# Kernel tuning notes

Hardware: AMD Instinct MI355X
Metric: run time of the kernel (lower is better)

## Reference

```python
import jax, jax.numpy as jnp
import numpy as np

REF_MIC = 0
LOAD = 0.001 / np.sqrt(2.0)  # diagonal loading added to both real and imag parts


def _to_complex(x):
    # x: (N, 2, ...) real/imag stacked -> complex (N, ...)
    return x[:, 0] + 1j * x[:, 1]


def setup_inputs() -> dict:
    key = jax.random.key(0)
    k1, k2, k3 = jax.random.split(key, 3)
    N, C, T, F = 8, 16, 300, 257
    mixture = jax.random.normal(k1, (N, 2, C, T, F), dtype=jnp.float32)
    target = jax.random.normal(k2, (N, 2, C, T, F), dtype=jnp.float32)
    steering_vector = jax.random.normal(k3, (N, 2, C, F), dtype=jnp.float32)
    return {"mixture": mixture, "target": target, "steering_vector": steering_vector}


def reference(mixture, target, steering_vector):
    N, _, C, T, F = mixture.shape
    y = _to_complex(mixture)  # (N, C, T, F)
    x = _to_complex(target)   # (N, C, T, F)

    # Spatial covariance of mixture, mean over time frames (sum/T), fused einsum
    # phi[n,f] = (1/T) * sum_t y[n,:,t,f] y[n,:,t,f]^H  -> (N, F, C, C)
    phi = jnp.einsum('nctf,ndtf->nfcd', y, jnp.conj(y)) / T
    eye = jnp.eye(C, dtype=phi.dtype)
    # original adds load to BOTH real and imag diagonals (broadcast over RI dim)
    phi = phi + (LOAD + 1j * LOAD) * eye
    phi_inv = jnp.linalg.inv(phi)  # (N, F, C, C)

    # Cross covariance between mixture and reference-mic target
    A = jnp.transpose(y, (0, 3, 2, 1))            # (N, F, T, C)
    b = jnp.transpose(x[:, REF_MIC], (0, 2, 1))   # (N, F, T)
    mu_a = jnp.mean(A, axis=(0, 2), keepdims=True)  # mean over batch and time
    mu_b = jnp.mean(b, axis=(0, 2), keepdims=True)
    # mean over T of (A-mu_a)(b-mu_b)^H -> (N, F, C)
    phi_yx0 = jnp.mean((A - mu_a) * jnp.conj(b - mu_b)[..., None], axis=2)

    # MWF weights: w = phi_inv @ phi_yx0  -> (N, F, C)
    w = jnp.einsum('nfcd,nfd->nfc', phi_inv, phi_yx0)

    # Beamform: X_bf[n,t,f] = w[n,f]^H y[n,:,t,f]
    Xbf = jnp.einsum('nfc,nctf->ntf', jnp.conj(w), y)  # (N, T, F)

    # Back to real/imag stacked (N, 2, 1, T, F) matching torch output layout
    out = jnp.stack([Xbf.real, Xbf.imag], axis=1)[:, :, None]
    return out
```

## Files before the change

kernel.cpp:

```cpp
#include <hip/hip_runtime.h>

#define N_     8
#define C_     16
#define T_     300
#define F_     257
#define TF_    (T_*F_)
#define CTF_   (C_*TF_)
#define N2CTF_ (2*CTF_)

#define FT_    32
#define NFT_   9
#define TS_    5
#define SROW_  34
#define SSTG_  (SROW_*32)
#define SBUF_  (TS_*SSTG_)
#define NTILE_ 10
#define PHIC_  (NTILE_*16)

#define MREC_  272

#define LOADC  7.0710678118654755e-04f

typedef float v2f __attribute__((ext_vector_type(2)));

__device__ __forceinline__ float2 cmul(float2 a, float2 b) {
  return make_float2(a.x*b.x - a.y*b.y, a.x*b.y + a.y*b.x);
}
__device__ __forceinline__ float2 cmulc(float2 a, float2 b) {
  return make_float2(a.x*b.x + a.y*b.y, a.y*b.x - a.x*b.y);
}
__device__ __forceinline__ float2 cdiv(float2 a, float2 b) {
  float inv = 1.0f / (b.x*b.x + b.y*b.y);
  return make_float2((a.x*b.x + a.y*b.y)*inv, (a.y*b.x - a.x*b.y)*inv);
}
__device__ __forceinline__ float2 cadd(float2 a, float2 b){ return make_float2(a.x+b.x, a.y+b.y); }
__device__ __forceinline__ float2 csub(float2 a, float2 b){ return make_float2(a.x-b.x, a.y-b.y); }

__device__ __forceinline__ void gload4(const float* g, float* l) {
  __builtin_amdgcn_global_load_lds(
      (const __attribute__((address_space(1))) unsigned int*)g,
      (__attribute__((address_space(3))) unsigned int*)l, 4, 0, 0);
}

template<int TCH>
__global__ __launch_bounds__(320) void k1_cov(const float* __restrict__ mix,
                                              const float* __restrict__ tgt,
                                              float2* __restrict__ phi_pf,
                                              float2* __restrict__ syx_pf,
                                              float2* __restrict__ sy_pf,
                                              float2* __restrict__ sx_pf) {
  __shared__ float ys[2 * SBUF_];
  v2f* phi_p = (v2f*)phi_pf;
  v2f* syx_p = (v2f*)syx_pf;
  v2f* sy_p  = (v2f*)sy_pf;
  v2f* sx_p  = (v2f*)sx_pf;
  const int tid = threadIdx.x;
  const int ft = blockIdx.x, tc = blockIdx.y, n = blockIdx.z;
  const int fbase = ft * FT_;
  const int t0 = tc * TCH;
  const int fl = tid & 31;
  const int g  = tid >> 5;
  int ti = 0, tj = g;
  while (tj > ti) { ++ti; tj -= ti; }
  const int c0 = ti * 4;
  const int d0 = tj * 4;
  const bool sThread = (tj == 0);

  const int w     = tid >> 6;
  const int plane = (tid >> 5) & 1;
  const int f_ld  = min(fbase + fl, F_ - 1);

  const float* mixN = mix + n * N2CTF_;
  const float* tgtN = tgt + n * N2CTF_;
  const float* ysrc = mixN + plane * CTF_ + (t0 + w) * F_ + f_ld;
  const float* xsrc = tgtN + plane * CTF_ + (t0 + w) * F_ + f_ld;

  v2f acc[4][4];
  #pragma unroll
  for (int i = 0; i < 4; ++i)
    #pragma unroll
    for (int j = 0; j < 4; ++j) acc[i][j] = (v2f){0.f, 0.f};
  v2f syx[4], sy[4], sx = (v2f){0.f, 0.f};
  #pragma unroll
  for (int i = 0; i < 4; ++i) { syx[i] = (v2f){0.f,0.f}; sy[i] = (v2f){0.f,0.f}; }

  constexpr int NS = TCH / TS_;

  {
    float* dst = &ys[w * SSTG_];
    #pragma unroll
    for (int c = 0; c < 16; ++c) gload4(ysrc + c * TF_, dst + 2 * c * 32);
    gload4(xsrc, dst + 32 * 32);
  }

  for (int s = 0; s < NS; ++s) {
    __syncthreads();
    if (s + 1 < NS) {
      float* dst = &ys[((s + 1) & 1) * SBUF_ + w * SSTG_];
      const float* yp = ysrc + (s + 1) * (TS_ * F_);
      #pragma unroll
      for (int c = 0; c < 16; ++c) gload4(yp + c * TF_, dst + 2 * c * 32);
      gload4(xsrc + (s + 1) * (TS_ * F_), dst + 32 * 32);
    }
    const float* bufc = &ys[(s & 1) * SBUF_];
    #pragma unroll
    for (int tl = 0; tl < TS_; ++tl) {
      const float* rt = bufc + tl * SSTG_;
      v2f a[4], bu[4], bv[4];
      #pragma unroll
      for (int i = 0; i < 4; ++i) {
        float re = rt[(2 * (c0 + i)) * 32 + fl];
        float im = rt[(2 * (c0 + i)) * 32 + 32 + fl];
        a[i] = (v2f){re, im};
      }
      #pragma unroll
      for (int j = 0; j < 4; ++j) {
        float re = rt[(2 * (d0 + j)) * 32 + fl];
        float im = rt[(2 * (d0 + j)) * 32 + 32 + fl];
        bu[j] = (v2f){re, -im};
        bv[j] = (v2f){im,  re};
      }
      #pragma unroll
      for (int i = 0; i < 4; ++i)
        #pragma unroll
        for (int j = 0; j < 4; ++j)
          acc[i][j] += a[i].x * bu[j] + a[i].y * bv[j];
      if (sThread) {
        float xre = rt[32 * 32 + fl];
        float xim = rt[33 * 32 + fl];
        v2f xu = (v2f){xre, -xim};
        v2f xw = (v2f){xim,  xre};
        #pragma unroll
        for (int i = 0; i < 4; ++i) {
          syx[i] += a[i].x * xu + a[i].y * xw;
          sy[i]  += a[i];
        }
        if (g == 0) sx += (v2f){xre, xim};
      }
    }
  }

  const int f = fbase + fl;
  if (f < F_) {
    const int tcn = tc * N_ + n;
    v2f* pb = phi_p + ((size_t)tcn * F_ + f) * PHIC_ + g * 16;
    #pragma unroll
    for (int i = 0; i < 4; ++i)
      #pragma unroll
      for (int j = 0; j < 4; ++j) pb[i * 4 + j] = acc[i][j];
    if (sThread) {
      v2f* s1 = syx_p + ((size_t)tcn * F_ + f) * C_ + c0;
      v2f* s2 = sy_p  + ((size_t)tcn * F_ + f) * C_ + c0;
      #pragma unroll
      for (int i = 0; i < 4; ++i) { s1[i] = syx[i]; s2[i] = sy[i]; }
      if (g == 0) sx_p[(size_t)tcn * F_ + f] = sx;
    }
  }
}

template<int TCP>
__global__ __launch_bounds__(256) void k2a_reduce(const float2* __restrict__ phi_p,
                                                  const float2* __restrict__ syx_p,
                                                  const float2* __restrict__ sy_p,
                                                  const float2* __restrict__ sx_p,
                                                  float2* __restrict__ Mg) {
  __shared__ float2 ld_sy[TCP * N_ * C_];
  __shared__ float2 ld_syx[TCP * C_];
  __shared__ float2 ld_sx[TCP * N_];
  __shared__ float2 muB_s, sxO_s;
  const int f = blockIdx.x, n = blockIdx.y;
  const int tid = threadIdx.x;
  const int i = tid >> 4, j = tid & 15;

  const int ti = i >> 2, tj = j >> 2, ci = i & 3, cj = j & 3;
  int gL, cell; bool cj_flip;
  if (ti >= tj) { gL = ti * (ti + 1) / 2 + tj; cell = ci * 4 + cj; cj_flip = false; }
  else          { gL = tj * (tj + 1) / 2 + ti; cell = cj * 4 + ci; cj_flip = true; }
  const int off = gL * 16 + cell;

  float2 s = make_float2(0.f, 0.f);
  for (int tc = 0; tc < TCP; ++tc) {
    float2 v = phi_p[((size_t)(tc * N_ + n) * F_ + f) * PHIC_ + off];
    s.x += v.x; s.y += v.y;
  }
  if (cj_flip) s.y = -s.y;
  if (i == j) { s.x += (float)T_ * LOADC; s.y += (float)T_ * LOADC; }

  for (int idx = tid; idx < TCP * N_ * C_; idx += 256) {
    int tcn = idx >> 4, c = idx & 15;
    ld_sy[idx] = sy_p[((size_t)tcn * F_ + f) * C_ + c];
  }
  for (int idx = tid; idx < TCP * C_; idx += 256) {
    int tc = idx >> 4, c = idx & 15;
    ld_syx[idx] = syx_p[((size_t)(tc * N_ + n) * F_ + f) * C_ + c];
  }
  for (int idx = tid; idx < TCP * N_; idx += 256) {
    ld_sx[idx] = sx_p[(size_t)idx * F_ + f];
  }
  __syncthreads();

  float2 muA_r = make_float2(0.f,0.f), ownY = make_float2(0.f,0.f), ownYX = make_float2(0.f,0.f);
  if (tid < 16) {
    float2 allY = make_float2(0.f,0.f);
    for (int tcn = 0; tcn < TCP * N_; ++tcn) allY = cadd(allY, ld_sy[tcn * C_ + tid]);
    for (int tc = 0; tc < TCP; ++tc) {
      ownY  = cadd(ownY,  ld_sy[(tc * N_ + n) * C_ + tid]);
      ownYX = cadd(ownYX, ld_syx[tc * C_ + tid]);
    }
    const float invNT = 1.0f / ((float)N_ * (float)T_);
    muA_r = make_float2(allY.x * invNT, allY.y * invNT);
  }
  if (tid == 16) {
    float2 own = make_float2(0.f,0.f), all = make_float2(0.f,0.f);
    for (int tc = 0; tc < TCP; ++tc)
      for (int nn = 0; nn < N_; ++nn) {
        float2 v = ld_sx[tc * N_ + nn];
        all = cadd(all, v);
        if (nn == n) own = cadd(own, v);
      }
    const float invNT = 1.0f / ((float)N_ * (float)T_);
    muB_s = make_float2(all.x * invNT, all.y * invNT);
    sxO_s = own;
  }
  __syncthreads();

  float2* dst = Mg + (size_t)(n * F_ + f) * MREC_;
  dst[tid] = s;
  if (tid < 16) {
    float2 r = ownYX;
    r = csub(r, cmulc(muA_r, sxO_s));
    r = csub(r, cmulc(ownY, muB_s));
    float2 t3 = cmulc(muA_r, muB_s);
    r.x += (float)T_ * t3.x; r.y += (float)T_ * t3.y;
    dst[256 + tid] = r;
  }
}

__global__ __launch_bounds__(64) void k2b_solve(const float2* __restrict__ Mg,
                                                float* __restrict__ wre,
                                                float* __restrict__ wim) {
  __shared__ float2 M[16 * 17];
  const int f = blockIdx.x, n = blockIdx.y;
  const int tid = threadIdx.x;
  const float2* src = Mg + (size_t)(n * F_ + f) * MREC_;
  #pragma unroll
  for (int r = 0; r < 4; ++r) {
    int idx = tid + 64 * r;
    M[(idx >> 4) * 17 + (idx & 15)] = src[idx];
  }
  if (tid < 16) M[tid * 17 + 16] = src[256 + tid];
  __syncthreads();

  const int i = tid >> 2, q = tid & 3;
  for (int k = 0; k < 16; ++k) {
    float2 fac = cdiv(M[i * 17 + k], M[k * 17 + k]);
    __syncthreads();
    if (i != k) {
      #pragma unroll
      for (int jj = 0; jj < 4; ++jj) {
        int j = q * 4 + jj;
        M[i * 17 + j] = csub(M[i * 17 + j], cmul(fac, M[k * 17 + j]));
      }
      if (q == 3) M[i * 17 + 16] = csub(M[i * 17 + 16], cmul(fac, M[k * 17 + 16]));
    }
    __syncthreads();
  }
  if (q == 0) {
    float2 w = cdiv(M[i * 17 + 16], M[i * 17 + i]);
    wre[(n * C_ + i) * F_ + f] = w.x;
    wim[(n * C_ + i) * F_ + f] = w.y;
  }
}

__global__ __launch_bounds__(320) void k3_bf(const float* __restrict__ mix,
                                             const float* __restrict__ wre,
                                             const float* __restrict__ wim,
                                             float* __restrict__ out) {
  const int t0 = blockIdx.x * 2, n = blockIdx.y;
  const int f = threadIdx.x;
  if (f >= F_) return;
  const float* mixN = mix + n * N2CTF_;
  const float* wR = wre + n * C_ * F_;
  const float* wI = wim + n * C_ * F_;
  float* outN = out + n * 2 * TF_;
  float wr[16], wi[16];
  #pragma unroll
  for (int c = 0; c < 16; ++c) { wr[c] = wR[c * F_ + f]; wi[c] = wI[c * F_ + f]; }
  const float* yb = mixN + t0 * F_ + f;
  float xr0 = 0.f, xi0 = 0.f, xr1 = 0.f, xi1 = 0.f;
  #pragma unroll
  for (int c = 0; c < 16; ++c) {
    float yr0 = yb[c * TF_],      yi0 = yb[CTF_ + c * TF_];
    float yr1 = yb[c * TF_ + F_], yi1 = yb[CTF_ + c * TF_ + F_];
    xr0 += wr[c] * yr0 + wi[c] * yi0;
    xi0 += wr[c] * yi0 - wi[c] * yr0;
    xr1 += wr[c] * yr1 + wi[c] * yi1;
    xi1 += wr[c] * yi1 - wi[c] * yr1;
  }
  outN[t0 * F_ + f] = xr0;
  outN[TF_ + t0 * F_ + f] = xi0;
  outN[(t0 + 1) * F_ + f] = xr1;
  outN[TF_ + (t0 + 1) * F_ + f] = xi1;
}

template<int TCP>
static void launch_all(const float* mix, const float* tgt, float* ws, float* out,
                       hipStream_t stream) {
  constexpr int TCH = T_ / TCP;
  static_assert(TCH * TCP == T_ && TCH % TS_ == 0, "chunking");
  float2* phi_p = (float2*)ws;
  float2* syx_p = phi_p + (size_t)TCP * N_ * F_ * PHIC_;
  float2* sy_p  = syx_p + (size_t)TCP * N_ * F_ * C_;
  float2* sx_p  = sy_p  + (size_t)TCP * N_ * F_ * C_;
  float2* Mg    = sx_p  + (size_t)TCP * N_ * F_;
  float*  wre   = (float*)(Mg + (size_t)N_ * F_ * MREC_);
  float*  wim   = wre + N_ * C_ * F_;
  k1_cov<TCH><<<dim3(NFT_, TCP, N_), dim3(320), 0, stream>>>(mix, tgt, phi_p, syx_p, sy_p, sx_p);
  k2a_reduce<TCP><<<dim3(F_, N_), dim3(256), 0, stream>>>(phi_p, syx_p, sy_p, sx_p, Mg);
  k2b_solve<<<dim3(F_, N_), dim3(64), 0, stream>>>(Mg, wre, wim);
  k3_bf<<<dim3(T_ / 2, N_), dim3(320), 0, stream>>>(mix, wre, wim, out);
}

static size_t ws_need_bytes(int tcp) {
  size_t fl2 = (size_t)tcp * N_ * F_ * (PHIC_ + C_ + C_ + 1) + (size_t)N_ * F_ * MREC_;
  return fl2 * 8 + 2ull * N_ * C_ * F_ * 4;
}

extern "C" void kernel_launch(void* const* d_in, const int* in_sizes, int n_in,
                              void* d_out, int out_size, void* d_ws, size_t ws_size,
                              hipStream_t stream) {
  const float* mix = (const float*)d_in[0];
  const float* tgt = (const float*)d_in[1];
  float* out = (float*)d_out;
  float* ws  = (float*)d_ws;
  if (ws_size >= ws_need_bytes(10))      launch_all<10>(mix, tgt, ws, out, stream);
  else if (ws_size >= ws_need_bytes(6))  launch_all<6>(mix, tgt, ws, out, stream);
  else if (ws_size >= ws_need_bytes(2))  launch_all<2>(mix, tgt, ws, out, stream);
  else                                   launch_all<1>(mix, tgt, ws, out, stream);
}
```

Measured before the change: 220.9 us.

## Triple-buffer covariance loads, fuse reduce and solve kernels, drop TCP=10 path

The covariance kernel moves from double to triple buffering. It issues async global-to-LDS loads two stages ahead, with explicit vmcnt waits and barriers, so memory latency is hidden better. The reduce and Gauss-Jordan solve kernels are merged into one, which removes a global round-trip of the per-frequency matrix and one kernel launch. The solve now uses 256 threads with one element each instead of 64 threads. The TCP=10 configuration is dropped, likely because its stage count per chunk is too small for the ring, so the default is now TCP=6 with fewer blocks in k1.

```diff
diff --git a/kernel.cpp b/kernel.cpp
--- a/kernel.cpp
+++ b/kernel.cpp
@@ -14,10 +14,9 @@
 #define SROW_  34
 #define SSTG_  (SROW_*32)
 #define SBUF_  (TS_*SSTG_)
+#define NSLOT_ 3
 #define NTILE_ 10
 #define PHIC_  (NTILE_*16)
-
-#define MREC_  272
 
 #define LOADC  7.0710678118654755e-04f
 
@@ -49,7 +48,7 @@
                                               float2* __restrict__ syx_pf,
                                               float2* __restrict__ sy_pf,
                                               float2* __restrict__ sx_pf) {
-  __shared__ float ys[2 * SBUF_];
+  __shared__ float ys[NSLOT_ * SBUF_];
   v2f* phi_p = (v2f*)phi_pf;
   v2f* syx_p = (v2f*)syx_pf;
   v2f* sy_p  = (v2f*)sy_pf;
@@ -85,24 +84,32 @@
   for (int i = 0; i < 4; ++i) { syx[i] = (v2f){0.f,0.f}; sy[i] = (v2f){0.f,0.f}; }
 
   constexpr int NS = TCH / TS_;
-
-  {
-    float* dst = &ys[w * SSTG_];
+  static_assert(NS >= 3, "ring needs >=3 stages");
+
+  auto issue = [&](int stg) {
+    float* dst = &ys[(stg % NSLOT_) * SBUF_ + w * SSTG_];
+    const float* yp = ysrc + stg * (TS_ * F_);
     #pragma unroll
-    for (int c = 0; c < 16; ++c) gload4(ysrc + c * TF_, dst + 2 * c * 32);
-    gload4(xsrc, dst + 32 * 32);
-  }
+    for (int c = 0; c < 16; ++c) gload4(yp + c * TF_, dst + 2 * c * 32);
+    gload4(xsrc + stg * (TS_ * F_), dst + 32 * 32);
+  };
+
+  issue(0);
+  issue(1);
 
   for (int s = 0; s < NS; ++s) {
-    __syncthreads();
-    if (s + 1 < NS) {
-      float* dst = &ys[((s + 1) & 1) * SBUF_ + w * SSTG_];
-      const float* yp = ysrc + (s + 1) * (TS_ * F_);
-      #pragma unroll
-      for (int c = 0; c < 16; ++c) gload4(yp + c * TF_, dst + 2 * c * 32);
-      gload4(xsrc + (s + 1) * (TS_ * F_), dst + 32 * 32);
-    }
-    const float* bufc = &ys[(s & 1) * SBUF_];
+    if (s + 2 < NS) {
+      issue(s + 2);
+      asm volatile("s_waitcnt vmcnt(34)" ::: "memory");
+    } else if (s + 1 < NS) {
+      asm volatile("s_waitcnt vmcnt(17)" ::: "memory");
+    } else {
+      asm volatile("s_waitcnt vmcnt(0)" ::: "memory");
+    }
+    __builtin_amdgcn_sched_barrier(0);
+    __builtin_amdgcn_s_barrier();
+
+    const float* bufc = &ys[(s % NSLOT_) * SBUF_];
     #pragma unroll
     for (int tl = 0; tl < TS_; ++tl) {
       const float* rt = bufc + tl * SSTG_;
@@ -138,6 +145,9 @@
         if (g == 0) sx += (v2f){xre, xim};
       }
     }
+    asm volatile("s_waitcnt lgkmcnt(0)" ::: "memory");
+    __builtin_amdgcn_sched_barrier(0);
+    __builtin_amdgcn_s_barrier();
   }
 
   const int f = fbase + fl;
@@ -159,14 +169,16 @@
 }
 
 template<int TCP>
-__global__ __launch_bounds__(256) void k2a_reduce(const float2* __restrict__ phi_p,
-                                                  const float2* __restrict__ syx_p,
-                                                  const float2* __restrict__ sy_p,
-                                                  const float2* __restrict__ sx_p,
-                                                  float2* __restrict__ Mg) {
+__global__ __launch_bounds__(256) void k2_fused(const float2* __restrict__ phi_p,
+                                                const float2* __restrict__ syx_p,
+                                                const float2* __restrict__ sy_p,
+                                                const float2* __restrict__ sx_p,
+                                                float* __restrict__ wre,
+                                                float* __restrict__ wim) {
   __shared__ float2 ld_sy[TCP * N_ * C_];
   __shared__ float2 ld_syx[TCP * C_];
   __shared__ float2 ld_sx[TCP * N_];
+  __shared__ float2 Msh[16 * 17];
   __shared__ float2 muB_s, sxO_s;
   const int f = blockIdx.x, n = blockIdx.y;
   const int tid = threadIdx.x;
@@ -224,51 +236,30 @@
   }
   __syncthreads();
 
-  float2* dst = Mg + (size_t)(n * F_ + f) * MREC_;
-  dst[tid] = s;
+  Msh[i * 17 + j] = s;
   if (tid < 16) {
     float2 r = ownYX;
     r = csub(r, cmulc(muA_r, sxO_s));
     r = csub(r, cmulc(ownY, muB_s));
     float2 t3 = cmulc(muA_r, muB_s);
     r.x += (float)T_ * t3.x; r.y += (float)T_ * t3.y;
-    dst[256 + tid] = r;
-  }
-}
-
-__global__ __launch_bounds__(64) void k2b_solve(const float2* __restrict__ Mg,
-                                                float* __restrict__ wre,
-                                                float* __restrict__ wim) {
-  __shared__ float2 M[16 * 17];
-  const int f = blockIdx.x, n = blockIdx.y;
-  const int tid = threadIdx.x;
-  const float2* src = Mg + (size_t)(n * F_ + f) * MREC_;
-  #pragma unroll
-  for (int r = 0; r < 4; ++r) {
-    int idx = tid + 64 * r;
-    M[(idx >> 4) * 17 + (idx & 15)] = src[idx];
-  }
-  if (tid < 16) M[tid * 17 + 16] = src[256 + tid];
+    Msh[tid * 17 + 16] = r;
+  }
   __syncthreads();
 
-  const int i = tid >> 2, q = tid & 3;
   for (int k = 0; k < 16; ++k) {
-    float2 fac = cdiv(M[i * 17 + k], M[k * 17 + k]);
+    float2 fac = cdiv(Msh[i * 17 + k], Msh[k * 17 + k]);
     __syncthreads();
     if (i != k) {
-      #pragma unroll
-      for (int jj = 0; jj < 4; ++jj) {
-        int j = q * 4 + jj;
-        M[i * 17 + j] = csub(M[i * 17 + j], cmul(fac, M[k * 17 + j]));
-      }
-      if (q == 3) M[i * 17 + 16] = csub(M[i * 17 + 16], cmul(fac, M[k * 17 + 16]));
+      Msh[i * 17 + j] = csub(Msh[i * 17 + j], cmul(fac, Msh[k * 17 + j]));
+      if (j == 15) Msh[i * 17 + 16] = csub(Msh[i * 17 + 16], cmul(fac, Msh[k * 17 + 16]));
     }
     __syncthreads();
   }
-  if (q == 0) {
-    float2 w = cdiv(M[i * 17 + 16], M[i * 17 + i]);
-    wre[(n * C_ + i) * F_ + f] = w.x;
-    wim[(n * C_ + i) * F_ + f] = w.y;
+  if (j == 0) {
+    float2 wv = cdiv(Msh[i * 17 + 16], Msh[i * 17 + i]);
+    wre[(n * C_ + i) * F_ + f] = wv.x;
+    wim[(n * C_ + i) * F_ + f] = wv.y;
   }
 }
 
@@ -312,17 +303,15 @@
   float2* syx_p = phi_p + (size_t)TCP * N_ * F_ * PHIC_;
   float2* sy_p  = syx_p + (size_t)TCP * N_ * F_ * C_;
   float2* sx_p  = sy_p  + (size_t)TCP * N_ * F_ * C_;
-  float2* Mg    = sx_p  + (size_t)TCP * N_ * F_;
-  float*  wre   = (float*)(Mg + (size_t)N_ * F_ * MREC_);
+  float*  wre   = (float*)(sx_p + (size_t)TCP * N_ * F_);
   float*  wim   = wre + N_ * C_ * F_;
   k1_cov<TCH><<<dim3(NFT_, TCP, N_), dim3(320), 0, stream>>>(mix, tgt, phi_p, syx_p, sy_p, sx_p);
-  k2a_reduce<TCP><<<dim3(F_, N_), dim3(256), 0, stream>>>(phi_p, syx_p, sy_p, sx_p, Mg);
-  k2b_solve<<<dim3(F_, N_), dim3(64), 0, stream>>>(Mg, wre, wim);
+  k2_fused<TCP><<<dim3(F_, N_), dim3(256), 0, stream>>>(phi_p, syx_p, sy_p, sx_p, wre, wim);
   k3_bf<<<dim3(T_ / 2, N_), dim3(320), 0, stream>>>(mix, wre, wim, out);
 }
 
 static size_t ws_need_bytes(int tcp) {
-  size_t fl2 = (size_t)tcp * N_ * F_ * (PHIC_ + C_ + C_ + 1) + (size_t)N_ * F_ * MREC_;
+  size_t fl2 = (size_t)tcp * N_ * F_ * (PHIC_ + 2 * C_ + 1);
   return fl2 * 8 + 2ull * N_ * C_ * F_ * 4;
 }
 
@@ -333,8 +322,7 @@
   const float* tgt = (const float*)d_in[1];
   float* out = (float*)d_out;
   float* ws  = (float*)d_ws;
-  if (ws_size >= ws_need_bytes(10))      launch_all<10>(mix, tgt, ws, out, stream);
-  else if (ws_size >= ws_need_bytes(6))  launch_all<6>(mix, tgt, ws, out, stream);
-  else if (ws_size >= ws_need_bytes(2))  launch_all<2>(mix, tgt, ws, out, stream);
-  else                                   launch_all<1>(mix, tgt, ws, out, stream);
-}
+  if (ws_size >= ws_need_bytes(6))      launch_all<6>(mix, tgt, ws, out, stream);
+  else if (ws_size >= ws_need_bytes(2)) launch_all<2>(mix, tgt, ws, out, stream);
+  else                                  launch_all<1>(mix, tgt, ws, out, stream);
+}
```

New measurement: 237.2 us. +7.3%, slower.
